# Optimization experiments

Hardware: AMD Instinct MI355X
Metric: run time of the kernel (lower is better)

The kernel has to match this reference:

```python
import jax, jax.numpy as jnp
import numpy as np

TEMPERATURE = 0.5
NEG_FILL = -9e15


def setup_inputs() -> dict:
    key = jax.random.key(0)
    k1, k2 = jax.random.split(key)
    B, D = 8192, 128
    z1 = jax.random.normal(k1, (B, D), dtype=jnp.float32)
    z2 = jax.random.normal(k2, (B, D), dtype=jnp.float32)
    return {"z1": z1, "z2": z2}


def reference(z1, z2):
    B = z1.shape[0]
    N = 2 * B
    z = jnp.concatenate([z1, z2], axis=0)              # [N, D]
    sim = jnp.matmul(z, z.T) / TEMPERATURE             # [N, N]
    eye = jnp.eye(N, dtype=bool)
    sim = jnp.where(eye, NEG_FILL, sim)
    idx = jnp.arange(N)
    pos_idx = (idx + B) % N
    positives = sim[idx, pos_idx]                      # [N]
    loss = -positives + jax.scipy.special.logsumexp(sim, axis=1)
    return loss.mean()
```

## Files before the change

### kernel.cpp

```cpp
#include <hip/hip_runtime.h>
#include <stdint.h>


typedef __attribute__((ext_vector_type(8))) short s16x8;
typedef __attribute__((ext_vector_type(16))) float f32x16;

#define N_TOT   16384
#define NHALF   8192
#define DDIM    128
#define NQ      12
#define TT      256
#define BN      64
#define BM      256
#define NRB     (N_TOT / BM)
#define CSH     128.0f
#define LN2     0.69314718055994530942f
#define BF_SCALE 1.6986436f

__device__ __forceinline__ unsigned short f2bf(float f) {
    union { float f; unsigned int u; } v; v.f = f;
    unsigned int u = v.u;
    unsigned int r = (u + 0x7FFFu + ((u >> 16) & 1u)) >> 16;
    return (unsigned short)r;
}

__device__ __forceinline__ void gload_lds16(const void* g, void* l) {
    __builtin_amdgcn_global_load_lds(
        (const __attribute__((address_space(1))) void*)g,
        (__attribute__((address_space(3))) void*)l, 16, 0, 0);
}

__global__ __launch_bounds__(256) void k_castpos(const float* __restrict__ z1,
                                                 const float* __restrict__ z2,
                                                 unsigned short* __restrict__ zb,
                                                 float* __restrict__ pos_part,
                                                 float* __restrict__ ws_acc) {
    __shared__ float red[4];
    int i = blockIdx.x * 256 + threadIdx.x;
    if (i == 0) { ws_acc[0] = 0.f; ((unsigned int*)ws_acc)[1] = 0u; }
    float4 a = ((const float4*)z1)[i];
    float4 b = ((const float4*)z2)[i];
    ushort4 oa, ob;
    oa.x = f2bf(a.x * BF_SCALE); oa.y = f2bf(a.y * BF_SCALE);
    oa.z = f2bf(a.z * BF_SCALE); oa.w = f2bf(a.w * BF_SCALE);
    ob.x = f2bf(b.x * BF_SCALE); ob.y = f2bf(b.y * BF_SCALE);
    ob.z = f2bf(b.z * BF_SCALE); ob.w = f2bf(b.w * BF_SCALE);
    ((ushort4*)zb)[i] = oa;
    ((ushort4*)(zb + (size_t)NHALF * DDIM))[i] = ob;
    float s = a.x * b.x + a.y * b.y + a.z * b.z + a.w * b.w;
    for (int o = 32; o; o >>= 1) s += __shfl_xor(s, o);
    int lane = threadIdx.x & 63, w = threadIdx.x >> 6;
    if (lane == 0) red[w] = s;
    __syncthreads();
    if (threadIdx.x == 0) pos_part[blockIdx.x] = red[0] + red[1] + red[2] + red[3];
}

__global__ __launch_bounds__(256) void k_main(const unsigned short* __restrict__ zb,
                                              float* __restrict__ ps) {
    __shared__ s16x8 tile[3][BN * 16];

    const int tid  = threadIdx.x;
    const int lane = tid & 63;
    const int w    = tid >> 6;
    const int h    = lane >> 5;
    const int l31  = lane & 31;

    const int bid = blockIdx.x;
    const int q   = bid >> 6;
    const int rb  = bid & 63;
    const int rowB   = rb * BM + w * 64;
    const int tstart = (q * TT) / NQ;
    const int ntile  = ((q + 1) * TT) / NQ - tstart;

    s16x8 rf0[8], rf1[8];
    {
        const s16x8* rp0 = (const s16x8*)(zb + (size_t)(rowB + l31) * DDIM);
        const s16x8* rp1 = (const s16x8*)(zb + (size_t)(rowB + 32 + l31) * DDIM);
        #pragma unroll
        for (int ks = 0; ks < 8; ++ks) { rf0[ks] = rp0[ks * 2 + h]; rf1[ks] = rp1[ks * 2 + h]; }
    }

    int soff[4];
    #pragma unroll
    for (int j = 0; j < 4; ++j) {
        int e = w * 4 + j;
        int col = e * 4 + (lane >> 4);
        int chunk = (lane & 15) ^ (col & 15);
        soff[j] = col * 256 + chunk * 16;
    }

    #pragma unroll
    for (int j = 0; j < 4; ++j)
        gload_lds16((const char*)zb + (size_t)tstart * 16384 + soff[j],
                    (char*)(&tile[0][0]) + (w * 4 + j) * 1024);
    #pragma unroll
    for (int j = 0; j < 4; ++j)
        gload_lds16((const char*)zb + (size_t)(tstart + 1) * 16384 + soff[j],
                    (char*)(&tile[1][0]) + (w * 4 + j) * 1024);

    float sa[4] = {0.f, 0.f, 0.f, 0.f};
    float sb[4] = {0.f, 0.f, 0.f, 0.f};

    int bc = 0;
    int bp = 2;
    for (int t = 0; t < ntile; ++t) {
        if (t < ntile - 1) asm volatile("s_waitcnt vmcnt(4)" ::: "memory");
        else               asm volatile("s_waitcnt vmcnt(0)" ::: "memory");
        __builtin_amdgcn_s_barrier();
        if (t + 2 < ntile) {
            #pragma unroll
            for (int j = 0; j < 4; ++j)
                gload_lds16((const char*)zb + (size_t)(tstart + t + 2) * 16384 + soff[j],
                            (char*)(&tile[0][0]) + bp * 16384 + (w * 4 + j) * 1024);
        }
        const int colBase = (tstart + t) * BN;
        const s16x8* tbase = &tile[0][0] + bc * (BN * 16);
        #pragma unroll
        for (int sdx = 0; sdx < 2; ++sdx) {
            const int c  = sdx * 32 + l31;
            const int cx = c & 15;
            const s16x8* tb = tbase + c * 16;
            s16x8 a[8];
            #pragma unroll
            for (int ks = 0; ks < 8; ++ks) a[ks] = tb[(ks * 2 + h) ^ cx];
            f32x16 acc0 = {-CSH, -CSH, -CSH, -CSH, -CSH, -CSH, -CSH, -CSH,
                           -CSH, -CSH, -CSH, -CSH, -CSH, -CSH, -CSH, -CSH};
            f32x16 acc1 = acc0;
            __builtin_amdgcn_s_setprio(1);
            #pragma unroll
            for (int ks = 0; ks < 8; ++ks) {
                acc0 = __builtin_amdgcn_mfma_f32_32x32x16_bf16(a[ks], rf0[ks], acc0, 0, 0, 0);
                acc1 = __builtin_amdgcn_mfma_f32_32x32x16_bf16(a[ks], rf1[ks], acc1, 0, 0, 0);
            }
            __builtin_amdgcn_s_setprio(0);
            const int cb = colBase + sdx * 32;
            if (cb == rowB) {
                #pragma unroll
                for (int r2 = 0; r2 < 16; ++r2) {
                    int crow = (r2 & 3) + 8 * (r2 >> 2) + 4 * h;
                    if (crow == l31) acc0[r2] = -1e30f;
                }
            }
            if (cb == rowB + 32) {
                #pragma unroll
                for (int r2 = 0; r2 < 16; ++r2) {
                    int crow = (r2 & 3) + 8 * (r2 >> 2) + 4 * h;
                    if (crow == l31) acc1[r2] = -1e30f;
                }
            }
            #pragma unroll
            for (int r2 = 0; r2 < 16; r2 += 4) {
                sa[0] += __builtin_amdgcn_exp2f(acc0[r2 + 0]);
                sa[1] += __builtin_amdgcn_exp2f(acc0[r2 + 1]);
                sa[2] += __builtin_amdgcn_exp2f(acc0[r2 + 2]);
                sa[3] += __builtin_amdgcn_exp2f(acc0[r2 + 3]);
                sb[0] += __builtin_amdgcn_exp2f(acc1[r2 + 0]);
                sb[1] += __builtin_amdgcn_exp2f(acc1[r2 + 1]);
                sb[2] += __builtin_amdgcn_exp2f(acc1[r2 + 2]);
                sb[3] += __builtin_amdgcn_exp2f(acc1[r2 + 3]);
            }
        }
        bc = (bc == 2) ? 0 : bc + 1;
        bp = (bp == 2) ? 0 : bp + 1;
    }

    float sA = (sa[0] + sa[1]) + (sa[2] + sa[3]);
    float sB = (sb[0] + sb[1]) + (sb[2] + sb[3]);
    sA += __shfl_xor(sA, 32);
    sB += __shfl_xor(sB, 32);
    if (lane < 32) {
        ps[(size_t)q * N_TOT + rowB + l31]      = sA;
        ps[(size_t)q * N_TOT + rowB + 32 + l31] = sB;
    }
}

__global__ __launch_bounds__(256) void k_cf(const float* __restrict__ ps,
                                            const float* __restrict__ pos_part,
                                            float* __restrict__ ws_acc,
                                            float* __restrict__ out) {
    __shared__ float red[4];
    __shared__ int last;
    const int tid = threadIdx.x;
    const int base = blockIdx.x * 1024;
    float ls = 0.f;
    #pragma unroll
    for (int k = 0; k < 4; ++k) {
        int row = base + k * 256 + tid;
        float s = 0.f;
        #pragma unroll
        for (int qq = 0; qq < NQ; ++qq) s += ps[(size_t)qq * N_TOT + row];
        ls += LN2 * (CSH + log2f(s));
    }
    for (int o = 32; o; o >>= 1) ls += __shfl_xor(ls, o);
    int lane = tid & 63, wv = tid >> 6;
    if (lane == 0) red[wv] = ls;
    __syncthreads();
    if (tid == 0) {
        atomicAdd(&ws_acc[0], red[0] + red[1] + red[2] + red[3]);
        __threadfence();
        unsigned int old = atomicAdd(&((unsigned int*)ws_acc)[1], 1u);
        last = (old == 15u) ? 1 : 0;
    }
    __syncthreads();
    if (last) {
        float p = pos_part[tid] + pos_part[tid + 256] +
                  pos_part[tid + 512] + pos_part[tid + 768];
        for (int o = 32; o; o >>= 1) p += __shfl_xor(p, o);
        if (lane == 0) red[wv] = p;
        __syncthreads();
        if (tid == 0) {
            float lse_tot = atomicAdd(&ws_acc[0], 0.f);
            float pos_tot = red[0] + red[1] + red[2] + red[3];
            out[0] = (lse_tot - 4.0f * pos_tot) * (1.0f / (float)N_TOT);
        }
    }
}

extern "C" void kernel_launch(void* const* d_in, const int* in_sizes, int n_in,
                              void* d_out, int out_size, void* d_ws, size_t ws_size,
                              hipStream_t stream) {
    const float* z1 = (const float*)d_in[0];
    const float* z2 = (const float*)d_in[1];
    float* out = (float*)d_out;

    char* ws = (char*)d_ws;
    float* ps       = (float*)ws;
    float* ws_acc   = (float*)(ws + (1u << 20));
    float* pos_part = (float*)(ws + (1u << 20) + 1024);
    unsigned short* zb = (unsigned short*)(ws + (2u << 20));

    k_castpos<<<dim3(1024), dim3(256), 0, stream>>>(z1, z2, zb, pos_part, ws_acc);
    k_main<<<dim3(NRB * NQ), dim3(256), 0, stream>>>(zb, ps);
    k_cf<<<dim3(16), dim3(256), 0, stream>>>(ps, pos_part, ws_acc, out);
}
```

Before: 138.6 us.

## Software-pipeline MFMA and exp stages, fuse final reduction, change column split

```diff
diff --git a/kernel.cpp b/kernel.cpp
--- a/kernel.cpp
+++ b/kernel.cpp
@@ -8,9 +8,9 @@
 #define N_TOT   16384
 #define NHALF   8192
 #define DDIM    128
-#define NQ      12
-#define TT      256
+#define NQ      8
 #define BN      64
+#define NTILE   32
 #define BM      256
 #define NRB     (N_TOT / BM)
 #define CSH     128.0f
@@ -34,10 +34,10 @@
                                                  const float* __restrict__ z2,
                                                  unsigned short* __restrict__ zb,
                                                  float* __restrict__ pos_part,
-                                                 float* __restrict__ ws_acc) {
+                                                 unsigned int* __restrict__ ctr) {
     __shared__ float red[4];
     int i = blockIdx.x * 256 + threadIdx.x;
-    if (i == 0) { ws_acc[0] = 0.f; ((unsigned int*)ws_acc)[1] = 0u; }
+    if (i == 0) ctr[0] = 0u;
     float4 a = ((const float4*)z1)[i];
     float4 b = ((const float4*)z2)[i];
     ushort4 oa, ob;
@@ -55,8 +55,48 @@
     if (threadIdx.x == 0) pos_part[blockIdx.x] = red[0] + red[1] + red[2] + red[3];
 }
 
+#define MFMA_SUB(TBASE, SDX, O0, O1) do {                                     \
+    const int c_  = (SDX) * 32 + l31;                                         \
+    const int cx_ = c_ & 15;                                                  \
+    const s16x8* tb_ = (TBASE) + c_ * 16;                                     \
+    O0 = acc_init; O1 = acc_init;                                             \
+    _Pragma("unroll")                                                         \
+    for (int ks_ = 0; ks_ < 8; ++ks_) {                                       \
+        s16x8 a_ = tb_[(ks_ * 2 + h) ^ cx_];                                  \
+        O0 = __builtin_amdgcn_mfma_f32_32x32x16_bf16(a_, rf0[ks_], O0, 0,0,0);\
+        O1 = __builtin_amdgcn_mfma_f32_32x32x16_bf16(a_, rf1[ks_], O1, 0,0,0);\
+    } } while (0)
+
+#define EXP_SUB(X0, X1, CB) do {                                              \
+    if ((CB) == rowB) {                                                       \
+        _Pragma("unroll")                                                     \
+        for (int r2_ = 0; r2_ < 16; ++r2_) {                                  \
+            int crow_ = (r2_ & 3) + 8 * (r2_ >> 2) + 4 * h;                   \
+            if (crow_ == l31) X0[r2_] = -1e30f;                               \
+        } }                                                                   \
+    if ((CB) == rowB + 32) {                                                  \
+        _Pragma("unroll")                                                     \
+        for (int r2_ = 0; r2_ < 16; ++r2_) {                                  \
+            int crow_ = (r2_ & 3) + 8 * (r2_ >> 2) + 4 * h;                   \
+            if (crow_ == l31) X1[r2_] = -1e30f;                               \
+        } }                                                                   \
+    _Pragma("unroll")                                                         \
+    for (int r2_ = 0; r2_ < 16; r2_ += 4) {                                   \
+        sa[0] += __builtin_amdgcn_exp2f(X0[r2_ + 0]);                         \
+        sa[1] += __builtin_amdgcn_exp2f(X0[r2_ + 1]);                         \
+        sa[2] += __builtin_amdgcn_exp2f(X0[r2_ + 2]);                         \
+        sa[3] += __builtin_amdgcn_exp2f(X0[r2_ + 3]);                         \
+        sb[0] += __builtin_amdgcn_exp2f(X1[r2_ + 0]);                         \
+        sb[1] += __builtin_amdgcn_exp2f(X1[r2_ + 1]);                         \
+        sb[2] += __builtin_amdgcn_exp2f(X1[r2_ + 2]);                         \
+        sb[3] += __builtin_amdgcn_exp2f(X1[r2_ + 3]);                         \
+    } } while (0)
+
 __global__ __launch_bounds__(256) void k_main(const unsigned short* __restrict__ zb,
-                                              float* __restrict__ ps) {
+                                              float* __restrict__ ps,
+                                              const float* __restrict__ pos_part,
+                                              unsigned int* __restrict__ ctr,
+                                              float* __restrict__ out) {
     __shared__ s16x8 tile[3][BN * 16];
 
     const int tid  = threadIdx.x;
@@ -69,8 +109,7 @@
     const int q   = bid >> 6;
     const int rb  = bid & 63;
     const int rowB   = rb * BM + w * 64;
-    const int tstart = (q * TT) / NQ;
-    const int ntile  = ((q + 1) * TT) / NQ - tstart;
+    const int tstart = q * NTILE;
 
     s16x8 rf0[8], rf1[8];
     {
@@ -98,71 +137,49 @@
         gload_lds16((const char*)zb + (size_t)(tstart + 1) * 16384 + soff[j],
                     (char*)(&tile[1][0]) + (w * 4 + j) * 1024);
 
+    const f32x16 acc_init = {-CSH, -CSH, -CSH, -CSH, -CSH, -CSH, -CSH, -CSH,
+                             -CSH, -CSH, -CSH, -CSH, -CSH, -CSH, -CSH, -CSH};
     float sa[4] = {0.f, 0.f, 0.f, 0.f};
     float sb[4] = {0.f, 0.f, 0.f, 0.f};
-
-    int bc = 0;
-    int bp = 2;
-    for (int t = 0; t < ntile; ++t) {
-        if (t < ntile - 1) asm volatile("s_waitcnt vmcnt(4)" ::: "memory");
+    f32x16 pA0, pA1, n0, n1, m0, m1;
+    int pcb;
+
+    asm volatile("s_waitcnt vmcnt(4)" ::: "memory");
+    __builtin_amdgcn_s_barrier();
+    #pragma unroll
+    for (int j = 0; j < 4; ++j)
+        gload_lds16((const char*)zb + (size_t)(tstart + 2) * 16384 + soff[j],
+                    (char*)(&tile[0][0]) + 2 * 16384 + (w * 4 + j) * 1024);
+    {
+        const s16x8* tbase = &tile[0][0];
+        MFMA_SUB(tbase, 0, n0, n1);
+        MFMA_SUB(tbase, 1, pA0, pA1);
+        EXP_SUB(n0, n1, tstart * BN);
+        pcb = tstart * BN + 32;
+    }
+
+    int bc = 1, bp = 0;
+    for (int t = 1; t < NTILE; ++t) {
+        if (t < NTILE - 1) asm volatile("s_waitcnt vmcnt(4)" ::: "memory");
         else               asm volatile("s_waitcnt vmcnt(0)" ::: "memory");
         __builtin_amdgcn_s_barrier();
-        if (t + 2 < ntile) {
+        if (t + 2 < NTILE) {
             #pragma unroll
             for (int j = 0; j < 4; ++j)
                 gload_lds16((const char*)zb + (size_t)(tstart + t + 2) * 16384 + soff[j],
                             (char*)(&tile[0][0]) + bp * 16384 + (w * 4 + j) * 1024);
         }
-        const int colBase = (tstart + t) * BN;
         const s16x8* tbase = &tile[0][0] + bc * (BN * 16);
-        #pragma unroll
-        for (int sdx = 0; sdx < 2; ++sdx) {
-            const int c  = sdx * 32 + l31;
-            const int cx = c & 15;
-            const s16x8* tb = tbase + c * 16;
-            s16x8 a[8];
-            #pragma unroll
-            for (int ks = 0; ks < 8; ++ks) a[ks] = tb[(ks * 2 + h) ^ cx];
-            f32x16 acc0 = {-CSH, -CSH, -CSH, -CSH, -CSH, -CSH, -CSH, -CSH,
-                           -CSH, -CSH, -CSH, -CSH, -CSH, -CSH, -CSH, -CSH};
-            f32x16 acc1 = acc0;
-            __builtin_amdgcn_s_setprio(1);
-            #pragma unroll
-            for (int ks = 0; ks < 8; ++ks) {
-                acc0 = __builtin_amdgcn_mfma_f32_32x32x16_bf16(a[ks], rf0[ks], acc0, 0, 0, 0);
-                acc1 = __builtin_amdgcn_mfma_f32_32x32x16_bf16(a[ks], rf1[ks], acc1, 0, 0, 0);
-            }
-            __builtin_amdgcn_s_setprio(0);
-            const int cb = colBase + sdx * 32;
-            if (cb == rowB) {
-                #pragma unroll
-                for (int r2 = 0; r2 < 16; ++r2) {
-                    int crow = (r2 & 3) + 8 * (r2 >> 2) + 4 * h;
-                    if (crow == l31) acc0[r2] = -1e30f;
-                }
-            }
-            if (cb == rowB + 32) {
-                #pragma unroll
-                for (int r2 = 0; r2 < 16; ++r2) {
-                    int crow = (r2 & 3) + 8 * (r2 >> 2) + 4 * h;
-                    if (crow == l31) acc1[r2] = -1e30f;
-                }
-            }
-            #pragma unroll
-            for (int r2 = 0; r2 < 16; r2 += 4) {
-                sa[0] += __builtin_amdgcn_exp2f(acc0[r2 + 0]);
-                sa[1] += __builtin_amdgcn_exp2f(acc0[r2 + 1]);
-                sa[2] += __builtin_amdgcn_exp2f(acc0[r2 + 2]);
-                sa[3] += __builtin_amdgcn_exp2f(acc0[r2 + 3]);
-                sb[0] += __builtin_amdgcn_exp2f(acc1[r2 + 0]);
-                sb[1] += __builtin_amdgcn_exp2f(acc1[r2 + 1]);
-                sb[2] += __builtin_amdgcn_exp2f(acc1[r2 + 2]);
-                sb[3] += __builtin_amdgcn_exp2f(acc1[r2 + 3]);
-            }
-        }
+        const int cb0 = (tstart + t) * BN;
+        MFMA_SUB(tbase, 0, n0, n1);
+        EXP_SUB(pA0, pA1, pcb);
+        MFMA_SUB(tbase, 1, m0, m1);
+        EXP_SUB(n0, n1, cb0);
+        pA0 = m0; pA1 = m1; pcb = cb0 + 32;
         bc = (bc == 2) ? 0 : bc + 1;
         bp = (bp == 2) ? 0 : bp + 1;
     }
+    EXP_SUB(pA0, pA1, pcb);
 
     float sA = (sa[0] + sa[1]) + (sa[2] + sa[3]);
     float sB = (sb[0] + sb[1]) + (sb[2] + sb[3]);
@@ -172,47 +189,39 @@
         ps[(size_t)q * N_TOT + rowB + l31]      = sA;
         ps[(size_t)q * N_TOT + rowB + 32 + l31] = sB;
     }
-}
-
-__global__ __launch_bounds__(256) void k_cf(const float* __restrict__ ps,
-                                            const float* __restrict__ pos_part,
-                                            float* __restrict__ ws_acc,
-                                            float* __restrict__ out) {
+
     __shared__ float red[4];
-    __shared__ int last;
-    const int tid = threadIdx.x;
-    const int base = blockIdx.x * 1024;
+    __shared__ int lastFlag;
+    __threadfence();
+    __syncthreads();
+    if (tid == 0) {
+        unsigned int old = atomicAdd(ctr, 1u);
+        lastFlag = (old == (unsigned)(NRB * NQ - 1)) ? 1 : 0;
+    }
+    __syncthreads();
+    if (!lastFlag) return;
+    __threadfence();
+
     float ls = 0.f;
-    #pragma unroll
-    for (int k = 0; k < 4; ++k) {
-        int row = base + k * 256 + tid;
+    for (int row = tid; row < N_TOT; row += 256) {
         float s = 0.f;
         #pragma unroll
         for (int qq = 0; qq < NQ; ++qq) s += ps[(size_t)qq * N_TOT + row];
-        ls += LN2 * (CSH + log2f(s));
+        ls += CSH + __builtin_amdgcn_logf(s);
     }
     for (int o = 32; o; o >>= 1) ls += __shfl_xor(ls, o);
-    int lane = tid & 63, wv = tid >> 6;
-    if (lane == 0) red[wv] = ls;
+    if (lane == 0) red[w] = ls;
+    __syncthreads();
+    float p = pos_part[tid] + pos_part[tid + 256] +
+              pos_part[tid + 512] + pos_part[tid + 768];
+    for (int o = 32; o; o >>= 1) p += __shfl_xor(p, o);
+    __shared__ float redp[4];
+    if (lane == 0) redp[w] = p;
     __syncthreads();
     if (tid == 0) {
-        atomicAdd(&ws_acc[0], red[0] + red[1] + red[2] + red[3]);
-        __threadfence();
-        unsigned int old = atomicAdd(&((unsigned int*)ws_acc)[1], 1u);
-        last = (old == 15u) ? 1 : 0;
-    }
-    __syncthreads();
-    if (last) {
-        float p = pos_part[tid] + pos_part[tid + 256] +
-                  pos_part[tid + 512] + pos_part[tid + 768];
-        for (int o = 32; o; o >>= 1) p += __shfl_xor(p, o);
-        if (lane == 0) red[wv] = p;
-        __syncthreads();
-        if (tid == 0) {
-            float lse_tot = atomicAdd(&ws_acc[0], 0.f);
-            float pos_tot = red[0] + red[1] + red[2] + red[3];
-            out[0] = (lse_tot - 4.0f * pos_tot) * (1.0f / (float)N_TOT);
-        }
+        float lse_tot = LN2 * (red[0] + red[1] + red[2] + red[3]);
+        float pos_tot = redp[0] + redp[1] + redp[2] + redp[3];
+        out[0] = (lse_tot - 4.0f * pos_tot) * (1.0f / (float)N_TOT);
     }
 }
 
@@ -224,12 +233,11 @@
     float* out = (float*)d_out;
 
     char* ws = (char*)d_ws;
-    float* ps       = (float*)ws;
-    float* ws_acc   = (float*)(ws + (1u << 20));
-    float* pos_part = (float*)(ws + (1u << 20) + 1024);
+    float* ps          = (float*)ws;
+    unsigned int* ctr  = (unsigned int*)(ws + (1u << 20));
+    float* pos_part    = (float*)(ws + (1u << 20) + 1024);
     unsigned short* zb = (unsigned short*)(ws + (2u << 20));
 
-    k_castpos<<<dim3(1024), dim3(256), 0, stream>>>(z1, z2, zb, pos_part, ws_acc);
-    k_main<<<dim3(NRB * NQ), dim3(256), 0, stream>>>(zb, ps);
-    k_cf<<<dim3(16), dim3(256), 0, stream>>>(ps, pos_part, ws_acc, out);
-}
+    k_castpos<<<dim3(1024), dim3(256), 0, stream>>>(z1, z2, zb, pos_part, ctr);
+    k_main<<<dim3(NRB * NQ), dim3(256), 0, stream>>>(zb, ps, pos_part, ctr, out);
+}
```

Result: slower. 207.4 us (+49.6%).
